# Performance work log

Measured on AMD Instinct MI355X. Metric: run time of the kernel, lower is better.

The kernel has to match this reference:

```python
import jax, jax.numpy as jnp
import numpy as np

B, N, E, M, H, OUT, F = 4, 10000, 160000, 4, 64, 64, 64


def setup_inputs() -> dict:
    key = jax.random.key(0)
    k1, k2, k3, k4, k5, k6 = jax.random.split(key, 6)
    node_fts = jax.random.normal(k1, (B, N, M, H), dtype=jnp.float32)
    hidden = jax.random.normal(k2, (B, N, M, H), dtype=jnp.float32)
    edge_fts = jax.random.normal(k3, (B, E, F), dtype=jnp.float32)
    edge_indices = jax.random.randint(k4, (B, E, 2), 0, N, dtype=jnp.int64)
    # hk.Linear params (truncated-normal-ish init approximated by scaled normal)
    W_nh = jax.random.normal(k5, (2 * H, OUT), dtype=jnp.float32) / np.sqrt(2 * H)
    b_nh = jnp.zeros((OUT,), dtype=jnp.float32)
    W_e = jax.random.normal(k6, (F, 1), dtype=jnp.float32) / np.sqrt(F)
    b_e = jnp.zeros((1,), dtype=jnp.float32)
    return {"node_fts": node_fts, "hidden": hidden, "edge_fts": edge_fts,
            "W_nh": W_nh, "b_nh": b_nh, "W_e": W_e, "b_e": b_e,
            "edge_indices": edge_indices}


def reference(node_fts, hidden, edge_fts, W_nh, b_nh, W_e, b_e, edge_indices):
    nb_nodes = node_fts.shape[1]
    src = edge_indices[..., 0]  # [B, E]
    tgt = edge_indices[..., 1]  # [B, E]
    # fuse node and hidden features, project: [B, N, M, 2H] @ [2H, OUT]
    nh = jnp.concatenate([node_fts, hidden], axis=-1)
    nh_fts = jnp.einsum('bnmc,co->bnmo', nh, W_nh) + b_nh  # [B, N, M, OUT]
    # gather per-edge source-node features along node axis
    nh_values = jnp.take_along_axis(nh_fts, src[:, :, None, None], axis=1)  # [B, E, M, OUT]
    # scalar gate per edge
    edge_coeff = jnp.einsum('bef,fo->beo', edge_fts, W_e) + b_e  # [B, E, 1]
    filtered = edge_coeff[..., None] * nh_values  # [B, E, M, OUT]
    # scatter-sum messages to target nodes, per batch element
    seg = jax.vmap(lambda d, s: jax.ops.segment_sum(d, s, num_segments=nb_nodes))
    updated_bits = seg(filtered, tgt)  # [B, N, M, OUT]
    return updated_bits
```

## Files before the change

kernel.cpp:

```cpp
#include <hip/hip_runtime.h>

#define Bc 4
#define Nc 10000
#define Ec 160000
#define NSEG (Bc * Nc)
#define NEDGE (Bc * Ec)
#define CAP 64
#define GATE_BLOCKS 2500
#define PROJ_BLOCKS 2500

typedef __attribute__((ext_vector_type(8))) short bf16x8;
typedef __attribute__((ext_vector_type(4))) float f32x4;

__device__ __forceinline__ unsigned short f2bf(float f) {
    union { float f; unsigned u; } x; x.f = f;
    return (unsigned short)((x.u + 0x7FFFu + ((x.u >> 16) & 1u)) >> 16);
}
__device__ __forceinline__ float bfhi(unsigned u) {
    union { unsigned u; float f; } x; x.u = u & 0xFFFF0000u; return x.f;
}
__device__ __forceinline__ float bflo(unsigned u) {
    union { unsigned u; float f; } x; x.u = u << 16; return x.f;
}

__device__ __forceinline__ float reduce16(float* p, int lane) {
#pragma unroll
    for (int off = 1, n = 8; off < 16; off <<= 1, n >>= 1) {
        const bool hi2 = (lane & off) != 0;
#pragma unroll
        for (int i = 0; i < 8; ++i)
            if (i < n) {
                const float keep = hi2 ? p[2 * i + 1] : p[2 * i];
                const float send = hi2 ? p[2 * i] : p[2 * i + 1];
                p[i] = keep + __shfl_xor(send, off, 64);
            }
    }
    return p[0];
}

__global__ __launch_bounds__(256) void proj_gate_kernel(
    const float* __restrict__ node, const float* __restrict__ hid,
    const float* __restrict__ Wnh, const float* __restrict__ bnh,
    unsigned short* __restrict__ nhf,
    const float* __restrict__ efts, const int* __restrict__ eidx,
    const float* __restrict__ We, const float* __restrict__ be,
    int2* __restrict__ epair, int slot_stride, int* __restrict__ cnt)
{
    __shared__ __align__(16) unsigned short wlds[8192];
    const int t = threadIdx.x;
    const int lane = t & 63;

    if (blockIdx.x >= GATE_BLOCKS) {
#pragma unroll
        for (int i = 0; i < 4; ++i) {
            const int f    = t + 256 * i;
            const int kt   = f >> 8;
            const int ct   = (f >> 6) & 3;
            const int l    = f & 63;
            const int quad = l >> 4, m = l & 15;
            const int col  = 16 * ct + m;
            const int krow = quad * 8 + 32 * kt;
            bf16x8 fr;
#pragma unroll
            for (int j = 0; j < 8; ++j)
                fr[j] = (short)f2bf(Wnh[(size_t)(krow + j) * 64 + col]);
            *(bf16x8*)(wlds + (size_t)f * 8) = fr;
        }
        __syncthreads();

        const int tile = (int)((blockIdx.x - GATE_BLOCKS) * 4 + (t >> 6));
        const int m    = lane & 15;
        const int quad = lane >> 4;

        float bias[4];
#pragma unroll
        for (int ct = 0; ct < 4; ++ct) bias[ct] = bnh[m + 16 * ct];

        const int arow = tile * 16 + m;
        f32x4 acc[4];
#pragma unroll
        for (int ct = 0; ct < 4; ++ct) acc[ct] = (f32x4){0.f, 0.f, 0.f, 0.f};

#pragma unroll
        for (int kt = 0; kt < 4; ++kt) {
            const int kbase = quad * 8 + 32 * kt;
            const float* pp = (kbase < 64)
                ? (node + (size_t)arow * 64 + kbase)
                : (hid  + (size_t)arow * 64 + (kbase - 64));
            const float4 lo = *(const float4*)pp;
            const float4 hi = *(const float4*)(pp + 4);
            bf16x8 a;
            a[0] = (short)f2bf(lo.x); a[1] = (short)f2bf(lo.y);
            a[2] = (short)f2bf(lo.z); a[3] = (short)f2bf(lo.w);
            a[4] = (short)f2bf(hi.x); a[5] = (short)f2bf(hi.y);
            a[6] = (short)f2bf(hi.z); a[7] = (short)f2bf(hi.w);
#pragma unroll
            for (int ct = 0; ct < 4; ++ct) {
                const bf16x8 bf = *(const bf16x8*)(wlds + (size_t)((kt * 4 + ct) * 64 + lane) * 8);
                acc[ct] = __builtin_amdgcn_mfma_f32_16x16x32_bf16(a, bf, acc[ct], 0, 0, 0);
            }
        }

        const int r0 = tile * 16 + quad * 4;
#pragma unroll
        for (int ct = 0; ct < 4; ++ct) {
            const int col = m + 16 * ct;
#pragma unroll
            for (int reg = 0; reg < 4; ++reg)
                nhf[(size_t)(r0 + reg) * 64 + col] = f2bf(acc[ct][reg] + bias[ct]);
        }
    } else {
        const int w  = (int)(blockIdx.x * 4 + (t >> 6));
        const int e0 = w * 64;
        const int b  = e0 / Ec;
        const int perm = 4 * (lane & 15) + (lane >> 4);

        const int2 st = *(const int2*)(eidx + (size_t)(e0 + perm) * 2);
        const int seg  = b * Nc + st.y;
        const int slot = atomicAdd(&cnt[seg], 1);

        const float4 w4 = *(const float4*)(We + (size_t)(lane & 15) * 4);
        const float* base = efts + (size_t)e0 * 64;
        float p[16];
#pragma unroll
        for (int j = 0; j < 16; ++j) {
            const float4 v = *(const float4*)(base + (size_t)j * 256 + lane * 4);
            p[j] = v.x * w4.x + v.y * w4.y + v.z * w4.z + v.w * w4.w;
        }
        const float cval = reduce16(p, lane) + be[0];
        if (slot < CAP)
            epair[(size_t)seg * slot_stride + slot] = make_int2(st.x, __float_as_int(cval));
    }
}

__global__ __launch_bounds__(256) void gather_kernel(
    const int* __restrict__ cnt, const int2* epair, int slot_stride,
    const unsigned* __restrict__ nhf, float* out)
{
    const int lane = threadIdx.x & 63;
    int pr = (int)((blockIdx.x * blockDim.x + threadIdx.x) >> 6);
    if (pr >= NSEG / 2) return;
    pr = __builtin_amdgcn_readfirstlane(pr);
    const int seg0 = pr * 2, seg1 = pr * 2 + 1;

    const int2* bp0 = epair + (size_t)seg0 * slot_stride;
    const int2* bp1 = epair + (size_t)seg1 * slot_stride;
    const int2 my0 = bp0[lane];
    const int2 my1 = bp1[lane];
    const int deg0 = cnt[seg0], deg1 = cnt[seg1];

#pragma unroll
    for (int s = 0; s < 2; ++s) {
        const int seg = s ? seg1 : seg0;
        const int deg = s ? deg1 : deg0;
        const int2 my = s ? my1 : my0;
        const int end = deg < CAP ? deg : CAP;
        const int b = seg / Nc;
        const unsigned* base = nhf + (size_t)b * Nc * 128 + lane * 2;

        f32x4 acc[4];
#pragma unroll
        for (int j = 0; j < 4; ++j) acc[j] = (f32x4){0.f, 0.f, 0.f, 0.f};

        int i = 0;
        for (; i + 8 <= end; i += 8) {
            int sx[8]; float cc[8]; uint2 r[8];
#pragma unroll
            for (int j = 0; j < 8; ++j) {
                sx[j] = __shfl(my.x, i + j, 64);
                cc[j] = __int_as_float(__shfl(my.y, i + j, 64));
            }
#pragma unroll
            for (int j = 0; j < 8; ++j) r[j] = *(const uint2*)(base + (size_t)sx[j] * 128);
#pragma unroll
            for (int j = 0; j < 8; ++j) {
                acc[j & 3][0] += cc[j] * bflo(r[j].x);
                acc[j & 3][1] += cc[j] * bfhi(r[j].x);
                acc[j & 3][2] += cc[j] * bflo(r[j].y);
                acc[j & 3][3] += cc[j] * bfhi(r[j].y);
            }
        }
        if (i + 4 <= end) {
            int sx[4]; float cc[4]; uint2 r[4];
#pragma unroll
            for (int j = 0; j < 4; ++j) {
                sx[j] = __shfl(my.x, i + j, 64);
                cc[j] = __int_as_float(__shfl(my.y, i + j, 64));
            }
#pragma unroll
            for (int j = 0; j < 4; ++j) r[j] = *(const uint2*)(base + (size_t)sx[j] * 128);
#pragma unroll
            for (int j = 0; j < 4; ++j) {
                acc[j][0] += cc[j] * bflo(r[j].x);
                acc[j][1] += cc[j] * bfhi(r[j].x);
                acc[j][2] += cc[j] * bflo(r[j].y);
                acc[j][3] += cc[j] * bfhi(r[j].y);
            }
            i += 4;
        }
        for (; i < end; ++i) {
            const int sx = __shfl(my.x, i, 64);
            const float cc = __int_as_float(__shfl(my.y, i, 64));
            const uint2 r = *(const uint2*)(base + (size_t)sx * 128);
            acc[0][0] += cc * bflo(r.x);
            acc[0][1] += cc * bfhi(r.x);
            acc[0][2] += cc * bflo(r.y);
            acc[0][3] += cc * bfhi(r.y);
        }
        float4 o;
        o.x = (acc[0][0] + acc[1][0]) + (acc[2][0] + acc[3][0]);
        o.y = (acc[0][1] + acc[1][1]) + (acc[2][1] + acc[3][1]);
        o.z = (acc[0][2] + acc[1][2]) + (acc[2][2] + acc[3][2]);
        o.w = (acc[0][3] + acc[1][3]) + (acc[2][3] + acc[3][3]);
        *(float4*)(out + (size_t)seg * 256 + lane * 4) = o;
    }
}

__global__ __launch_bounds__(256) void edge_atomic_kernel(
    const float* __restrict__ efts, const int* __restrict__ eidx,
    const float* __restrict__ We, const float* __restrict__ be,
    const unsigned* __restrict__ nhf, float* __restrict__ out)
{
    const int lane = threadIdx.x & 63;
    const int eg   = (int)((blockIdx.x * blockDim.x + threadIdx.x) >> 6);
    if (eg >= NEDGE) return;
    const int b = eg / Ec;
    float c = efts[(size_t)eg * 64 + lane] * We[lane];
#pragma unroll
    for (int off = 32; off > 0; off >>= 1) c += __shfl_xor(c, off, 64);
    c += be[0];
    const int src = eidx[(size_t)eg * 2 + 0];
    const int tgt = eidx[(size_t)eg * 2 + 1];
    const uint2 r = *(const uint2*)(nhf + ((size_t)(b * Nc + src)) * 128 + lane * 2);
    float* op = out + ((size_t)(b * Nc + tgt)) * 256 + lane * 4;
    atomicAdd(op + 0, c * bflo(r.x));
    atomicAdd(op + 1, c * bfhi(r.x));
    atomicAdd(op + 2, c * bflo(r.y));
    atomicAdd(op + 3, c * bfhi(r.y));
}

extern "C" void kernel_launch(void* const* d_in, const int* in_sizes, int n_in,
                              void* d_out, int out_size, void* d_ws, size_t ws_size,
                              hipStream_t stream) {
    const float* node = (const float*)d_in[0];
    const float* hid  = (const float*)d_in[1];
    const float* efts = (const float*)d_in[2];
    const float* Wnh  = (const float*)d_in[3];
    const float* bnh  = (const float*)d_in[4];
    const float* We   = (const float*)d_in[5];
    const float* be   = (const float*)d_in[6];
    const int*   eidx = (const int*)d_in[7];
    float* out = (float*)d_out;

    unsigned* ws = (unsigned*)d_ws;
    unsigned short* nhf16 = (unsigned short*)ws;
    int* cnt = (int*)(ws + 5120000);
    const size_t ws_compact = (size_t)10280000 * 4;
    const size_t ws_minimal = (size_t)5160000 * 4;

    if (ws_size >= ws_minimal) {
        int2* epair;
        int stride;
        if (ws_size >= ws_compact) { epair = (int2*)(ws + 5160000); stride = 64; }
        else                       { epair = (int2*)d_out;          stride = 128; }
        hipMemsetAsync(cnt, 0, (size_t)NSEG * sizeof(int), stream);
        proj_gate_kernel<<<GATE_BLOCKS + PROJ_BLOCKS, 256, 0, stream>>>(
            node, hid, Wnh, bnh, nhf16, efts, eidx, We, be, epair, stride, cnt);
        gather_kernel<<<NSEG / 8, 256, 0, stream>>>(cnt, epair, stride, (const unsigned*)ws, out);
    } else {
        proj_gate_kernel<<<GATE_BLOCKS + PROJ_BLOCKS, 256, 0, stream>>>(
            node, hid, Wnh, bnh, nhf16, efts, eidx, We, be,
            (int2*)d_out , 128, (int*)d_out );
        hipMemsetAsync(d_out, 0, (size_t)out_size * sizeof(float), stream);
        edge_atomic_kernel<<<NEDGE / 4, 256, 0, stream>>>(efts, eidx, We, be, (const unsigned*)ws, out);
    }
}
```

Before: 352.2 us.

## Use persistent grid-stride waves with double-buffered loads in proj/gate kernel

```diff
diff --git a/kernel.cpp b/kernel.cpp
--- a/kernel.cpp
+++ b/kernel.cpp
@@ -6,8 +6,12 @@
 #define NSEG (Bc * Nc)
 #define NEDGE (Bc * Ec)
 #define CAP 64
-#define GATE_BLOCKS 2500
-#define PROJ_BLOCKS 2500
+#define NCHUNK 10000
+#define NTILE 10000
+#define GATE_BLOCKS 480
+#define PROJ_BLOCKS 288
+#define GATE_WAVES (GATE_BLOCKS * 4)
+#define PROJ_WAVES (PROJ_BLOCKS * 4)
 
 typedef __attribute__((ext_vector_type(8))) short bf16x8;
 typedef __attribute__((ext_vector_type(4))) float f32x4;
@@ -38,7 +42,7 @@
     return p[0];
 }
 
-__global__ __launch_bounds__(256) void proj_gate_kernel(
+__global__ __launch_bounds__(256, 3) void proj_gate_kernel(
     const float* __restrict__ node, const float* __restrict__ hid,
     const float* __restrict__ Wnh, const float* __restrict__ bnh,
     unsigned short* __restrict__ nhf,
@@ -68,68 +72,112 @@
         }
         __syncthreads();
 
-        const int tile = (int)((blockIdx.x - GATE_BLOCKS) * 4 + (t >> 6));
         const int m    = lane & 15;
         const int quad = lane >> 4;
-
         float bias[4];
 #pragma unroll
         for (int ct = 0; ct < 4; ++ct) bias[ct] = bnh[m + 16 * ct];
 
-        const int arow = tile * 16 + m;
-        f32x4 acc[4];
-#pragma unroll
-        for (int ct = 0; ct < 4; ++ct) acc[ct] = (f32x4){0.f, 0.f, 0.f, 0.f};
-
-#pragma unroll
-        for (int kt = 0; kt < 4; ++kt) {
-            const int kbase = quad * 8 + 32 * kt;
-            const float* pp = (kbase < 64)
-                ? (node + (size_t)arow * 64 + kbase)
-                : (hid  + (size_t)arow * 64 + (kbase - 64));
-            const float4 lo = *(const float4*)pp;
-            const float4 hi = *(const float4*)(pp + 4);
-            bf16x8 a;
-            a[0] = (short)f2bf(lo.x); a[1] = (short)f2bf(lo.y);
-            a[2] = (short)f2bf(lo.z); a[3] = (short)f2bf(lo.w);
-            a[4] = (short)f2bf(hi.x); a[5] = (short)f2bf(hi.y);
-            a[6] = (short)f2bf(hi.z); a[7] = (short)f2bf(hi.w);
+        auto pissue = [&](float4* lo, float4* hi, int tt) {
+            const size_t arow = (size_t)tt * 16 + m;
+#pragma unroll
+            for (int kt = 0; kt < 4; ++kt) {
+                const int kbase = quad * 8 + 32 * kt;
+                const float* pp = (kbase < 64)
+                    ? (node + arow * 64 + kbase)
+                    : (hid  + arow * 64 + (kbase - 64));
+                lo[kt] = *(const float4*)pp;
+                hi[kt] = *(const float4*)(pp + 4);
+            }
+        };
+        auto pfinish = [&](const float4* lo, const float4* hi, int tt) {
+            f32x4 acc[4];
+#pragma unroll
+            for (int ct = 0; ct < 4; ++ct) acc[ct] = (f32x4){0.f, 0.f, 0.f, 0.f};
+#pragma unroll
+            for (int kt = 0; kt < 4; ++kt) {
+                bf16x8 a;
+                a[0] = (short)f2bf(lo[kt].x); a[1] = (short)f2bf(lo[kt].y);
+                a[2] = (short)f2bf(lo[kt].z); a[3] = (short)f2bf(lo[kt].w);
+                a[4] = (short)f2bf(hi[kt].x); a[5] = (short)f2bf(hi[kt].y);
+                a[6] = (short)f2bf(hi[kt].z); a[7] = (short)f2bf(hi[kt].w);
+#pragma unroll
+                for (int ct = 0; ct < 4; ++ct) {
+                    const bf16x8 bf = *(const bf16x8*)(wlds + (size_t)((kt * 4 + ct) * 64 + lane) * 8);
+                    acc[ct] = __builtin_amdgcn_mfma_f32_16x16x32_bf16(a, bf, acc[ct], 0, 0, 0);
+                }
+            }
+            const int r0 = tt * 16 + quad * 4;
 #pragma unroll
             for (int ct = 0; ct < 4; ++ct) {
-                const bf16x8 bf = *(const bf16x8*)(wlds + (size_t)((kt * 4 + ct) * 64 + lane) * 8);
-                acc[ct] = __builtin_amdgcn_mfma_f32_16x16x32_bf16(a, bf, acc[ct], 0, 0, 0);
-            }
-        }
-
-        const int r0 = tile * 16 + quad * 4;
-#pragma unroll
-        for (int ct = 0; ct < 4; ++ct) {
-            const int col = m + 16 * ct;
-#pragma unroll
-            for (int reg = 0; reg < 4; ++reg)
-                nhf[(size_t)(r0 + reg) * 64 + col] = f2bf(acc[ct][reg] + bias[ct]);
+                const int col = m + 16 * ct;
+#pragma unroll
+                for (int reg = 0; reg < 4; ++reg)
+                    nhf[(size_t)(r0 + reg) * 64 + col] = f2bf(acc[ct][reg] + bias[ct]);
+            }
+        };
+
+        int tt = (int)((blockIdx.x - GATE_BLOCKS) * 4 + (t >> 6));
+        if (tt >= NTILE) return;
+        float4 loA[4], hiA[4], loB[4], hiB[4];
+        pissue(loA, hiA, tt);
+        while (true) {
+            int tn = tt + PROJ_WAVES;
+            if (tn < NTILE) {
+                pissue(loB, hiB, tn);
+                pfinish(loA, hiA, tt);
+                tt = tn;
+                tn = tt + PROJ_WAVES;
+                if (tn < NTILE) {
+                    pissue(loA, hiA, tn);
+                    pfinish(loB, hiB, tt);
+                    tt = tn;
+                } else { pfinish(loB, hiB, tt); break; }
+            } else { pfinish(loA, hiA, tt); break; }
         }
     } else {
-        const int w  = (int)(blockIdx.x * 4 + (t >> 6));
-        const int e0 = w * 64;
-        const int b  = e0 / Ec;
         const int perm = 4 * (lane & 15) + (lane >> 4);
-
-        const int2 st = *(const int2*)(eidx + (size_t)(e0 + perm) * 2);
-        const int seg  = b * Nc + st.y;
-        const int slot = atomicAdd(&cnt[seg], 1);
-
         const float4 w4 = *(const float4*)(We + (size_t)(lane & 15) * 4);
-        const float* base = efts + (size_t)e0 * 64;
-        float p[16];
-#pragma unroll
-        for (int j = 0; j < 16; ++j) {
-            const float4 v = *(const float4*)(base + (size_t)j * 256 + lane * 4);
-            p[j] = v.x * w4.x + v.y * w4.y + v.z * w4.z + v.w * w4.w;
-        }
-        const float cval = reduce16(p, lane) + be[0];
-        if (slot < CAP)
-            epair[(size_t)seg * slot_stride + slot] = make_int2(st.x, __float_as_int(cval));
+        const float be0 = be[0];
+
+        auto gissue = [&](float4* v, int2& st, int c) {
+            const float* base = efts + (size_t)c * 64 * 64;
+#pragma unroll
+            for (int j = 0; j < 16; ++j)
+                v[j] = *(const float4*)(base + (size_t)j * 256 + lane * 4);
+            st = *(const int2*)(eidx + (size_t)(c * 64 + perm) * 2);
+        };
+        auto gfinish = [&](const float4* v, int2 st, int c) {
+            const int b = (c * 64) / Ec;
+            const int seg = b * Nc + st.y;
+            const int slot = atomicAdd(&cnt[seg], 1);
+            float p[16];
+#pragma unroll
+            for (int j = 0; j < 16; ++j)
+                p[j] = v[j].x * w4.x + v[j].y * w4.y + v[j].z * w4.z + v[j].w * w4.w;
+            const float cval = reduce16(p, lane) + be0;
+            if (slot < CAP)
+                epair[(size_t)seg * slot_stride + slot] = make_int2(st.x, __float_as_int(cval));
+        };
+
+        int c = (int)(blockIdx.x * 4 + (t >> 6));
+        if (c >= NCHUNK) return;
+        float4 vA[16], vB[16]; int2 stA, stB;
+        gissue(vA, stA, c);
+        while (true) {
+            int cn = c + GATE_WAVES;
+            if (cn < NCHUNK) {
+                gissue(vB, stB, cn);
+                gfinish(vA, stA, c);
+                c = cn;
+                cn = c + GATE_WAVES;
+                if (cn < NCHUNK) {
+                    gissue(vA, stA, cn);
+                    gfinish(vB, stB, c);
+                    c = cn;
+                } else { gfinish(vB, stB, c); break; }
+            } else { gfinish(vA, stA, c); break; }
+        }
     }
 }
 
```

New measurement: 360.6 us. 1.02x slower.
